# Optimization experiments

Hardware: AMD Instinct MI355X
Metric: run time of the kernel (lower is better)

Reference implementation:

```python
import jax, jax.numpy as jnp
import numpy as np

B, S, D, H = 2, 2048, 1024, 16
DH = D // H  # head dim = 64


def _split_heads(x):
    # [B,S,D] -> [B,H,S,DH]
    return x.reshape(B, S, H, DH).transpose(0, 2, 1, 3)


def setup_inputs() -> dict:
    key = jax.random.key(0)
    ks = jax.random.split(key, 14)
    sc = 1.0 / np.sqrt(D)
    p = {"hidden_states": jax.random.normal(ks[0], (B, S, D), jnp.float32)}
    names = ["Wq", "Wk1", "Wk2", "Wv1", "Wv2", "Wd"]
    for i, n in enumerate(names):
        p[n] = jax.random.normal(ks[1 + 2 * i], (D, D), jnp.float32) * sc
        p["b" + n[1:]] = jax.random.normal(ks[2 + 2 * i], (D,), jnp.float32) * 0.02
    return p


def reference(hidden_states, Wq, bq, Wk1, bk1, Wk2, bk2, Wv1, bv1, Wv2, bv2, Wd, bd):
    q = _split_heads(hidden_states @ Wq + bq)
    k1 = _split_heads(hidden_states @ Wk1 + bk1)
    k2 = _split_heads(hidden_states @ Wk2 + bk2)
    v1 = _split_heads(hidden_states @ Wv1 + bv1)
    v2 = _split_heads(hidden_states @ Wv2 + bv2)

    scores = jnp.einsum("bhqd,bhkd->bhqk", q, k1) / np.sqrt(DH)
    causal = jnp.tril(jnp.ones((S, S), dtype=bool))  # True = keep
    scores = jnp.where(causal, scores, -jnp.inf)
    probs = jax.nn.softmax(scores, axis=-1)

    ctx = jnp.einsum("bhqk,bhkd->bhqd", probs, v1)          # [B,H,S,DH]
    ctx = jnp.einsum("bhqd,bhkd->bhqk", ctx, k2)            # [B,H,S,S]
    ctx = jnp.einsum("bhqk,bhkd->bhqd", ctx, v2)            # [B,H,S,DH]

    ctx = ctx.transpose(0, 2, 1, 3).reshape(B, S, D)
    return ctx @ Wd + bd
```

## Files before the change

kernel.cpp:

```cpp
#include <hip/hip_runtime.h>
#include <hip/hip_bf16.h>

typedef __bf16 bf16x8 __attribute__((ext_vector_type(8)));
typedef float f32x4 __attribute__((ext_vector_type(4)));
using bf16 = __hip_bfloat16;

#define SEQ 2048
#define DM 1024
#define NH 16
#define DH 64
#define NBH 32
#define MR 4096

#define WAITBAR(N) asm volatile("s_waitcnt vmcnt(" #N ")\n\ts_barrier" ::: "memory")

static __device__ __forceinline__ void async_cp16(const void* gsrc, void* ldsdst) {
  __builtin_amdgcn_global_load_lds((__attribute__((address_space(1))) void*)gsrc,
                                   (__attribute__((address_space(3))) void*)ldsdst, 16, 0, 0);
}

static __device__ __forceinline__ unsigned short f2bfu(float f) {
  bf16 h = __float2bfloat16(f);
  unsigned short u; __builtin_memcpy(&u, &h, 2); return u;
}
static __device__ __forceinline__ unsigned int pack_bf2(float lo, float hi) {
  return (unsigned int)f2bfu(lo) | ((unsigned int)f2bfu(hi) << 16);
}

__global__ __launch_bounds__(256) void cast_x(const float* __restrict__ X, bf16* __restrict__ Xb) {
  long g = ((long)blockIdx.x * 256 + threadIdx.x) * 8;
  float4 a = *(const float4*)(X + g);
  float4 b = *(const float4*)(X + g + 4);
  unsigned short u[8];
  u[0]=f2bfu(a.x); u[1]=f2bfu(a.y); u[2]=f2bfu(a.z); u[3]=f2bfu(a.w);
  u[4]=f2bfu(b.x); u[5]=f2bfu(b.y); u[6]=f2bfu(b.z); u[7]=f2bfu(b.w);
  uint4 o; __builtin_memcpy(&o, u, 16);
  *(uint4*)(Xb + g) = o;
}

struct WPtrs { const float* w[6]; };

__global__ __launch_bounds__(256) void transpose_cast_w(WPtrs wp, bf16* __restrict__ WtAll) {
  const int z = blockIdx.z;
  const float* W = wp.w[z];
  bf16* Wt = WtAll + (long)z * DM * DM;
  __shared__ float Ts[32][33];
  int n0 = blockIdx.x * 32, k0 = blockIdx.y * 32;
  int tx = threadIdx.x, ty = threadIdx.y;
#pragma unroll
  for (int it = 0; it < 4; ++it)
    Ts[ty + 8*it][tx] = W[(long)(k0 + ty + 8*it) * DM + n0 + tx];
  __syncthreads();
#pragma unroll
  for (int it = 0; it < 4; ++it)
    Wt[(long)(n0 + ty + 8*it) * DM + k0 + tx] = __float2bfloat16(Ts[tx][ty + 8*it]);
}

struct ProjArgs {
  const float* bias[5];
  bf16* out[5];
};

__global__ __launch_bounds__(256, 2) void gemm_proj(const bf16* __restrict__ A,
                                                    const bf16* __restrict__ WtAll, ProjArgs p) {
  __shared__ alignas(16) bf16 SM[36864];
  bf16* As = SM;
  bf16* Bs = SM + 12288;
  const int tid = threadIdx.x;
  const int bid = blockIdx.x;
  const int mt = bid & 31, nt = bid >> 5;
  const int m0 = mt * 128;
  const int z = nt >> 2;
  const int n0z = (nt & 3) * 256;
  const bf16* Bt = WtAll + (long)z * DM * DM + (long)n0z * DM;

  const int wave = tid >> 6, lane = tid & 63, l15 = lane & 15, l4 = lane >> 4;
  const int wm = wave >> 1, wn = wave & 1;

  const int prow = tid >> 2;
  const int cc = (tid & 3) ^ ((prow >> 1) & 3);
  const bf16* sA0 = A  + (long)(m0 + prow) * DM + cc * 8;
  const bf16* sA1 = sA0 + 64L * DM;
  const bf16* sB0 = Bt + (long)prow * DM + cc * 8;
  const bf16* sB1 = sB0 + 64L * DM;
  const bf16* sB2 = sB0 + 128L * DM;
  const bf16* sB3 = sB0 + 192L * DM;
  char* dA = (char*)As + wave * 1024;
  char* dB = (char*)Bs + wave * 1024;

#define PSTAGE(KT_, BUF_) do {                                  \
    int ko_ = (KT_) * 32;                                       \
    async_cp16(sA0 + ko_, dA + (BUF_) * 8192);                  \
    async_cp16(sA1 + ko_, dA + (BUF_) * 8192 + 4096);           \
    async_cp16(sB0 + ko_, dB + (BUF_) * 16384);                 \
    async_cp16(sB1 + ko_, dB + (BUF_) * 16384 + 4096);          \
    async_cp16(sB2 + ko_, dB + (BUF_) * 16384 + 8192);          \
    async_cp16(sB3 + ko_, dB + (BUF_) * 16384 + 12288);         \
  } while (0)

  const int slot8 = (l4 ^ ((l15 >> 1) & 3)) * 8;
  const int arow = wm * 64 + l15;
  const int brow = wn * 128 + l15;
  f32x4 acc[4][8] = {};

#define PCOMPUTE(BUF_) do {                                                        \
    const bf16* ab_ = As + (BUF_) * 4096;                                          \
    const bf16* bb_ = Bs + (BUF_) * 8192;                                          \
    bf16x8 af_[4], bq_[8];                                                         \
    _Pragma("unroll")                                                              \
    for (int i = 0; i < 4; ++i) af_[i] = *(const bf16x8*)(ab_ + (arow + i * 16) * 32 + slot8); \
    _Pragma("unroll")                                                              \
    for (int j = 0; j < 8; ++j) bq_[j] = *(const bf16x8*)(bb_ + (brow + j * 16) * 32 + slot8); \
    _Pragma("unroll")                                                              \
    for (int i = 0; i < 4; ++i)                                                    \
      _Pragma("unroll")                                                            \
      for (int j = 0; j < 8; ++j)                                                  \
        acc[i][j] = __builtin_amdgcn_mfma_f32_16x16x32_bf16(af_[i], bq_[j], acc[i][j], 0, 0, 0); \
  } while (0)

  PSTAGE(0, 0);
  PSTAGE(1, 1);
  int buf = 0;
#pragma unroll 1
  for (int k = 0; k < 31; ++k) {
    WAITBAR(6);
    if (k < 30) {
      int nb = buf + 2; if (nb > 2) nb -= 3;
      PSTAGE(k + 2, nb);
    }
    PCOMPUTE(buf);
    ++buf; if (buf > 2) buf = 0;
  }
  WAITBAR(0);
  PCOMPUTE(buf);
#undef PSTAGE
#undef PCOMPUTE

  const float* bias = p.bias[z];
  bf16* out = p.out[z];
  float bv[8];
#pragma unroll
  for (int j = 0; j < 8; ++j) bv[j] = bias[n0z + wn * 128 + j * 16 + l15];

  if (z < 2) {
    const float scale = (z == 0) ? 0.125f * 1.44269504f : 1.0f;
#pragma unroll
    for (int i = 0; i < 4; ++i)
#pragma unroll
      for (int j = 0; j < 8; ++j)
#pragma unroll
        for (int r = 0; r < 4; ++r) {
          int m = m0 + wm * 64 + i * 16 + l4 * 4 + r;
          int n = n0z + wn * 128 + j * 16 + l15;
          int b = m >> 11, s = m & 2047, hh = n >> 6, d = n & 63;
          out[((long)((b * NH + hh) * SEQ + s)) * DH + d] =
              __float2bfloat16((acc[i][j][r] + bv[j]) * scale);
        }
  } else {
    __syncthreads();
    bf16* Os = SM;
#pragma unroll
    for (int i = 0; i < 4; ++i)
#pragma unroll
      for (int j = 0; j < 8; ++j)
#pragma unroll
        for (int r = 0; r < 4; ++r) {
          int nl = wn * 128 + j * 16 + l15;
          int ml = wm * 64 + i * 16 + l4 * 4 + r;
          Os[nl * 136 + ml] = __float2bfloat16(acc[i][j][r] + bv[j]);
        }
    __syncthreads();
    {
      int nl = tid;
      int ng = n0z + nl;
      int hh = ng >> 6, d = ng & 63;
      int b = m0 >> 11, s0 = m0 & 2047;
      bf16* op = out + ((long)((b * NH + hh) * DH + d)) * SEQ + s0;
#pragma unroll
      for (int u = 0; u < 16; ++u)
        *(bf16x8*)(op + u * 8) = *(const bf16x8*)(Os + nl * 136 + u * 8);
    }
  }
}

static __device__ __forceinline__ void gemm_core128(
    const bf16* __restrict__ A, const bf16* __restrict__ Bt,
    bf16* As, bf16* Bs, f32x4 (&acc)[4][4], int m0, int tid)
{
  const int wave = tid >> 6, lane = tid & 63, l15 = lane & 15, l4 = lane >> 4;
  const int wm = wave >> 1, wn = wave & 1;
  const int r0 = tid >> 2;
  const int c0 = (tid & 3) ^ ((r0 >> 1) & 3);
  const bf16* srcA0 = A + (long)(m0 + r0) * DM + c0 * 8;
  const bf16* srcA1 = A + (long)(m0 + r0 + 64) * DM + c0 * 8;
  const bf16* srcB0 = Bt + (long)r0 * DM + c0 * 8;
  const bf16* srcB1 = Bt + (long)(r0 + 64) * DM + c0 * 8;
  char* dstA = (char*)As + wave * 1024;
  char* dstB = (char*)Bs + wave * 1024;

#define STAGE(KT_, BUF_) do {                                   \
    int ko_ = (KT_) * 32;                                       \
    int bo_ = (BUF_) * 8192;                                    \
    async_cp16(srcA0 + ko_, dstA + bo_);                        \
    async_cp16(srcA1 + ko_, dstA + bo_ + 4096);                 \
    async_cp16(srcB0 + ko_, dstB + bo_);                        \
    async_cp16(srcB1 + ko_, dstB + bo_ + 4096);                 \
  } while (0)

  const int slot8 = (l4 ^ ((l15 >> 1) & 3)) * 8;
  const int arow = wm * 64 + l15;
  const int brow = wn * 64 + l15;

#define COMPUTE(BUF_) do {                                                         \
    const bf16* ab_ = As + (BUF_) * 4096;                                          \
    const bf16* bb_ = Bs + (BUF_) * 4096;                                          \
    bf16x8 af_[4], bq_[4];                                                         \
    _Pragma("unroll")                                                              \
    for (int i = 0; i < 4; ++i) af_[i] = *(const bf16x8*)(ab_ + (arow + i * 16) * 32 + slot8); \
    _Pragma("unroll")                                                              \
    for (int j = 0; j < 4; ++j) bq_[j] = *(const bf16x8*)(bb_ + (brow + j * 16) * 32 + slot8); \
    _Pragma("unroll")                                                              \
    for (int i = 0; i < 4; ++i)                                                    \
      _Pragma("unroll")                                                            \
      for (int j = 0; j < 4; ++j)                                                  \
        acc[i][j] = __builtin_amdgcn_mfma_f32_16x16x32_bf16(af_[i], bq_[j], acc[i][j], 0, 0, 0); \
  } while (0)

  STAGE(0, 0);
  STAGE(1, 1);
  int buf = 0;
#pragma unroll 1
  for (int k = 0; k < 31; ++k) {
    WAITBAR(4);
    if (k < 30) {
      int nb = buf + 2; if (nb > 2) nb -= 3;
      STAGE(k + 2, nb);
    }
    COMPUTE(buf);
    ++buf; if (buf > 2) buf = 0;
  }
  WAITBAR(0);
  COMPUTE(buf);
#undef STAGE
#undef COMPUTE
}

__global__ __launch_bounds__(256, 3) void gemm_out(const bf16* __restrict__ A, const bf16* __restrict__ Bt,
                                                   const float* __restrict__ bias, float* __restrict__ out) {
  __shared__ alignas(16) bf16 As[3 * 128 * 32];
  __shared__ alignas(16) bf16 Bs[3 * 128 * 32];
  const int tid = threadIdx.x;
  const int bid = blockIdx.x;
  const int nt = bid & 7, mt = bid >> 3;
  const int m0 = mt * 128, n0 = nt * 128;
  f32x4 acc[4][4] = {};
  gemm_core128(A, Bt + (long)n0 * DM, As, Bs, acc, m0, tid);
  const int wave = tid >> 6, lane = tid & 63, l15 = lane & 15, l4 = lane >> 4;
  const int wm = wave >> 1, wn = wave & 1;
  float bv[4];
#pragma unroll
  for (int j = 0; j < 4; ++j) bv[j] = bias[n0 + wn * 64 + j * 16 + l15];
#pragma unroll
  for (int i = 0; i < 4; ++i)
#pragma unroll
    for (int j = 0; j < 4; ++j)
#pragma unroll
      for (int r = 0; r < 4; ++r) {
        int m = m0 + wm * 64 + i * 16 + l4 * 4 + r;
        int n = n0 + wn * 64 + j * 16 + l15;
        out[(long)m * DM + n] = acc[i][j][r] + bv[j];
      }
}

__global__ __launch_bounds__(256) void m_kernel(
    const bf16* __restrict__ k2t, const bf16* __restrict__ v2t, float* __restrict__ Mbuf)
{
  const int scx = blockIdx.x;
  const int bh = blockIdx.y;
  const int tid = threadIdx.x, wave = tid >> 6, lane = tid & 63, l15 = lane & 15, l4 = lane >> 4;
  const bf16* kp = k2t + (long)bh * DH * SEQ;
  const bf16* vp = v2t + (long)bh * DH * SEQ;
  __shared__ alignas(16) bf16 K2s[64 * 32];
  __shared__ alignas(16) bf16 V2s[64 * 32];
  f32x4 acc[4] = {};
  const int s0 = scx * 256;
  for (int kk = 0; kk < 256; kk += 32) {
    __syncthreads();
    {
      int c = tid, r = c >> 2, pp = c & 3;
      async_cp16(kp + (long)r * SEQ + s0 + kk + pp * 8, K2s + wave * 64 * 8);
      async_cp16(vp + (long)r * SEQ + s0 + kk + pp * 8, V2s + wave * 64 * 8);
    }
    __syncthreads();
    int arow = 16 * wave + l15;
    bf16x8 a = *(const bf16x8*)(K2s + arow * 32 + l4 * 8);
#pragma unroll
    for (int nb = 0; nb < 4; ++nb) {
      int col = nb * 16 + l15;
      bf16x8 b = *(const bf16x8*)(V2s + col * 32 + l4 * 8);
      acc[nb] = __builtin_amdgcn_mfma_f32_16x16x32_bf16(a, b, acc[nb], 0, 0, 0);
    }
  }
  float* Mp = Mbuf + (long)bh * 4096;
#pragma unroll
  for (int nb = 0; nb < 4; ++nb)
#pragma unroll
    for (int r = 0; r < 4; ++r) {
      int row = 16 * wave + l4 * 4 + r;
      int col = nb * 16 + l15;
      atomicAdd(Mp + row * 64 + col, acc[nb][r]);
    }
}

static __device__ __forceinline__ void redist(const unsigned int (&pk)[4][2], bf16x8 (&pb)[2],
                                              int l4, int l15) {
#pragma unroll
  for (int h = 0; h < 2; ++h) {
    unsigned int w4[4];
#pragma unroll
    for (int w = 0; w < 4; ++w) {
      int src = l15 + 16 * (2 * (l4 & 1) + (w >> 1));
      unsigned int va = (unsigned int)__shfl((int)pk[2 * h][w & 1], src);
      unsigned int vb = (unsigned int)__shfl((int)pk[2 * h + 1][w & 1], src);
      w4[w] = (l4 & 2) ? vb : va;
    }
    __builtin_memcpy(&pb[h], w4, 16);
  }
}

__global__ __launch_bounds__(256) void attn_fused(
    const bf16* __restrict__ q,
    const bf16* __restrict__ k1,
    const bf16* __restrict__ v1t,
    const float* __restrict__ Mbuf,
    bf16* __restrict__ ctx2,
    unsigned int* __restrict__ cnt)
{
  const int tid = threadIdx.x, wave = tid >> 6, lane = tid & 63;
  const int l15 = lane & 15, l4 = lane >> 4;

  __shared__ alignas(16) bf16 Ks[2][64 * 64];
  __shared__ alignas(16) bf16 Vs[2][64 * 64];
  __shared__ int ts;

#define STAGE_KV(JJ, BUF) do {                                                     \
    int kv0_ = 64 * (JJ);                                                          \
    int c_ = tid, row_ = c_ >> 3, ch_ = c_ & 7;                                    \
    async_cp16(kp + (long)(kv0_ + row_) * DH + ((ch_ ^ (row_ & 7)) * 8),           \
               (char*)Ks[BUF] + wave * 1024);                                      \
    async_cp16(vp + (long)row_ * SEQ + kv0_ + ((ch_ ^ (row_ & 7)) * 8),            \
               (char*)Vs[BUF] + wave * 1024);                                      \
    c_ = tid + 256; row_ = c_ >> 3; ch_ = c_ & 7;                                  \
    async_cp16(kp + (long)(kv0_ + row_) * DH + ((ch_ ^ (row_ & 7)) * 8),           \
               (char*)Ks[BUF] + 4096 + wave * 1024);                               \
    async_cp16(vp + (long)row_ * SEQ + kv0_ + ((ch_ ^ (row_ & 7)) * 8),            \
               (char*)Vs[BUF] + 4096 + wave * 1024);                               \
  } while (0)

#pragma unroll 1
  for (;;) {
    if (tid == 0) ts = (int)atomicAdd(cnt, 1u);
    __syncthreads();
    const int t = ts;
    if (t >= 1024) break;
    const int tq = 31 - (t >> 5);
    const int bh = t & 31;
    const int bb = bh >> 4, hh = bh & 15;
    const bf16* qp = q   + (long)bh * SEQ * DH;
    const bf16* kp = k1  + (long)bh * SEQ * DH;
    const bf16* vp = v1t + (long)bh * DH * SEQ;
    const float* Mp = Mbuf + (long)bh * 4096;

    bf16x8 mf[4][2];
#pragma unroll
    for (int db = 0; db < 4; ++db)
#pragma unroll
      for (int h = 0; h < 2; ++h) {
        bf16x8 tt;
#pragma unroll
        for (int j = 0; j < 8; ++j)
          tt[j] = (__bf16)Mp[(32 * h + 8 * l4 + j) * 64 + 16 * db + l15];
        mf[db][h] = tt;
      }

    const int Q0 = 64 * tq;
    const int qg = Q0 + 16 * wave + l15;
    const int jmax = tq;

    STAGE_KV(0, 0);

    bf16x8 aq[2];
#pragma unroll
    for (int h = 0; h < 2; ++h)
      aq[h] = *(const bf16x8*)(qp + (long)qg * DH + 32 * h + 8 * l4);

    float m_run = -__builtin_inff(), l_run = 0.f;
    f32x4 acc_o[4] = {};

    __syncthreads();

#pragma unroll 1
    for (int j = 0; j <= jmax; ++j) {
      const int cur = j & 1;
      if (j < jmax) STAGE_KV(j + 1, cur ^ 1);

      f32x4 sc[4] = {};
      __builtin_amdgcn_s_setprio(1);
#pragma unroll
      for (int nb = 0; nb < 4; ++nb) {
        const bf16* krow = Ks[cur] + (16 * nb + l15) * 64;
#pragma unroll
        for (int h = 0; h < 2; ++h) {
          bf16x8 kf = *(const bf16x8*)(krow + (((4 * h + l4) ^ (l15 & 7)) * 8));
          sc[nb] = __builtin_amdgcn_mfma_f32_16x16x32_bf16(kf, aq[h], sc[nb], 0, 0, 0);
        }
      }
      __builtin_amdgcn_s_setprio(0);

      if (j == jmax) {
        const int kv0 = 64 * j;
#pragma unroll
        for (int nb = 0; nb < 4; ++nb)
#pragma unroll
          for (int r = 0; r < 4; ++r)
            if (kv0 + 16 * nb + 4 * l4 + r > qg) sc[nb][r] = -__builtin_inff();
      }

      float tmax = -__builtin_inff();
#pragma unroll
      for (int nb = 0; nb < 4; ++nb)
#pragma unroll
        for (int r = 0; r < 4; ++r) tmax = fmaxf(tmax, sc[nb][r]);
      tmax = fmaxf(tmax, __shfl_xor(tmax, 16));
      tmax = fmaxf(tmax, __shfl_xor(tmax, 32));

      float mnew = m_run;
      if (!__all(tmax <= m_run)) {
        mnew = fmaxf(m_run, tmax);
        float sf = __builtin_amdgcn_exp2f(m_run - mnew);
        m_run = mnew;
        l_run *= sf;
#pragma unroll
        for (int db = 0; db < 4; ++db)
#pragma unroll
          for (int r = 0; r < 4; ++r) acc_o[db][r] *= sf;
      }

      float ssum = 0.f;
      unsigned int pk[4][2];
#pragma unroll
      for (int nb = 0; nb < 4; ++nb)
#pragma unroll
        for (int pr = 0; pr < 2; ++pr) {
          float p0 = __builtin_amdgcn_exp2f(sc[nb][2 * pr]     - m_run);
          float p1 = __builtin_amdgcn_exp2f(sc[nb][2 * pr + 1] - m_run);
          ssum += p0 + p1;
          pk[nb][pr] = pack_bf2(p0, p1);
        }
      ssum += __shfl_xor(ssum, 16);
      ssum += __shfl_xor(ssum, 32);
      l_run += ssum;

      bf16x8 pb[2];
      redist(pk, pb, l4, l15);
      __builtin_amdgcn_s_setprio(1);
#pragma unroll
      for (int db = 0; db < 4; ++db) {
        const bf16* vrow = Vs[cur] + (16 * db + l15) * 64;
#pragma unroll
        for (int h = 0; h < 2; ++h) {
          bf16x8 vf = *(const bf16x8*)(vrow + (((4 * h + l4) ^ (l15 & 7)) * 8));
          acc_o[db] = __builtin_amdgcn_mfma_f32_16x16x32_bf16(vf, pb[h], acc_o[db], 0, 0, 0);
        }
      }
      __builtin_amdgcn_s_setprio(0);
      __syncthreads();
    }

    float invl = __builtin_amdgcn_rcpf(l_run);
    unsigned int ck[4][2];
#pragma unroll
    for (int db = 0; db < 4; ++db)
#pragma unroll
      for (int pr = 0; pr < 2; ++pr)
        ck[db][pr] = pack_bf2(acc_o[db][2 * pr] * invl, acc_o[db][2 * pr + 1] * invl);
    bf16x8 cb[2];
    redist(ck, cb, l4, l15);
    f32x4 o2[4] = {};
#pragma unroll
    for (int db = 0; db < 4; ++db)
#pragma unroll
      for (int h = 0; h < 2; ++h)
        o2[db] = __builtin_amdgcn_mfma_f32_16x16x32_bf16(mf[db][h], cb[h], o2[db], 0, 0, 0);

    bf16* Os = (bf16*)Ks;
#pragma unroll
    for (int db = 0; db < 4; ++db)
#pragma unroll
      for (int r = 0; r < 4; ++r)
        Os[(16 * wave + l15) * 72 + 16 * db + 4 * l4 + r] = __float2bfloat16(o2[db][r]);
    __syncthreads();
    {
      int rr = tid >> 2, cc2 = tid & 3;
      long obase = ((long)(bb * SEQ + Q0 + rr)) * DM + hh * DH + cc2 * 16;
      *(bf16x8*)(ctx2 + obase)     = *(const bf16x8*)(Os + rr * 72 + cc2 * 16);
      *(bf16x8*)(ctx2 + obase + 8) = *(const bf16x8*)(Os + rr * 72 + cc2 * 16 + 8);
    }
  }
#undef STAGE_KV
}

extern "C" void kernel_launch(void* const* d_in, const int* in_sizes, int n_in,
                              void* d_out, int out_size, void* d_ws, size_t ws_size,
                              hipStream_t stream) {
  (void)in_sizes; (void)n_in; (void)out_size; (void)ws_size;
  const float* X = (const float*)d_in[0];
  const float* W[6]    = {(const float*)d_in[1], (const float*)d_in[3], (const float*)d_in[5],
                          (const float*)d_in[7], (const float*)d_in[9], (const float*)d_in[11]};
  const float* bias[6] = {(const float*)d_in[2], (const float*)d_in[4], (const float*)d_in[6],
                          (const float*)d_in[8], (const float*)d_in[10], (const float*)d_in[12]};

  char* ws = (char*)d_ws;
  bf16* Xb  = (bf16*)(ws);
  bf16* Wt  = (bf16*)(ws + (8L  << 20));
  bf16* qB  = (bf16*)(ws + (20L << 20));
  bf16* k1B = (bf16*)(ws + (28L << 20));
  bf16* k2t = (bf16*)(ws + (36L << 20));
  bf16* v1t = (bf16*)(ws + (44L << 20));
  bf16* v2t = (bf16*)(ws + (52L << 20));
  float* Mb = (float*)(ws + (60L << 20));
  unsigned int* cnt = (unsigned int*)(ws + (61L << 20));
  bf16* c2  = Xb;

  cast_x<<<2048, 256, 0, stream>>>(X, Xb);

  WPtrs wp; for (int z = 0; z < 6; ++z) wp.w[z] = W[z];
  transpose_cast_w<<<dim3(32, 32, 6), dim3(32, 8), 0, stream>>>(wp, Wt);

  ProjArgs pa;
  for (int z = 0; z < 5; ++z) pa.bias[z] = bias[z];
  pa.out[0] = qB; pa.out[1] = k1B; pa.out[2] = k2t; pa.out[3] = v1t; pa.out[4] = v2t;
  gemm_proj<<<640, 256, 0, stream>>>(Xb, Wt, pa);

  hipMemsetAsync(Mb, 0, ((size_t)1 << 20) + 64, stream);
  hipMemsetAsync(cnt, 0, 4, stream);
  m_kernel<<<dim3(8, 32), 256, 0, stream>>>(k2t, v2t, Mb);

  attn_fused<<<512, 256, 0, stream>>>(qB, k1B, v1t, Mb, c2, cnt);

  gemm_out<<<256, 256, 0, stream>>>(c2, Wt + 5L * DM * DM, bias[5], (float*)d_out);
}
```

Measured before the change: 171.2 us.

## Rewrite fused attention as per-wave 32-row tiles with 32x32 MFMA and register-streamed K/V

```diff
diff --git a/kernel.cpp b/kernel.cpp
--- a/kernel.cpp
+++ b/kernel.cpp
@@ -3,6 +3,7 @@
 
 typedef __bf16 bf16x8 __attribute__((ext_vector_type(8)));
 typedef float f32x4 __attribute__((ext_vector_type(4)));
+typedef float f32x16 __attribute__((ext_vector_type(16)));
 using bf16 = __hip_bfloat16;
 
 #define SEQ 2048
@@ -312,22 +313,6 @@
     }
 }
 
-static __device__ __forceinline__ void redist(const unsigned int (&pk)[4][2], bf16x8 (&pb)[2],
-                                              int l4, int l15) {
-#pragma unroll
-  for (int h = 0; h < 2; ++h) {
-    unsigned int w4[4];
-#pragma unroll
-    for (int w = 0; w < 4; ++w) {
-      int src = l15 + 16 * (2 * (l4 & 1) + (w >> 1));
-      unsigned int va = (unsigned int)__shfl((int)pk[2 * h][w & 1], src);
-      unsigned int vb = (unsigned int)__shfl((int)pk[2 * h + 1][w & 1], src);
-      w4[w] = (l4 & 2) ? vb : va;
-    }
-    __builtin_memcpy(&pb[h], w4, 16);
-  }
-}
-
 __global__ __launch_bounds__(256) void attn_fused(
     const bf16* __restrict__ q,
     const bf16* __restrict__ k1,
@@ -336,178 +321,207 @@
     bf16* __restrict__ ctx2,
     unsigned int* __restrict__ cnt)
 {
-  const int tid = threadIdx.x, wave = tid >> 6, lane = tid & 63;
-  const int l15 = lane & 15, l4 = lane >> 4;
-
-  __shared__ alignas(16) bf16 Ks[2][64 * 64];
-  __shared__ alignas(16) bf16 Vs[2][64 * 64];
-  __shared__ int ts;
-
-#define STAGE_KV(JJ, BUF) do {                                                     \
-    int kv0_ = 64 * (JJ);                                                          \
-    int c_ = tid, row_ = c_ >> 3, ch_ = c_ & 7;                                    \
-    async_cp16(kp + (long)(kv0_ + row_) * DH + ((ch_ ^ (row_ & 7)) * 8),           \
-               (char*)Ks[BUF] + wave * 1024);                                      \
-    async_cp16(vp + (long)row_ * SEQ + kv0_ + ((ch_ ^ (row_ & 7)) * 8),            \
-               (char*)Vs[BUF] + wave * 1024);                                      \
-    c_ = tid + 256; row_ = c_ >> 3; ch_ = c_ & 7;                                  \
-    async_cp16(kp + (long)(kv0_ + row_) * DH + ((ch_ ^ (row_ & 7)) * 8),           \
-               (char*)Ks[BUF] + 4096 + wave * 1024);                               \
-    async_cp16(vp + (long)row_ * SEQ + kv0_ + ((ch_ ^ (row_ & 7)) * 8),            \
-               (char*)Vs[BUF] + 4096 + wave * 1024);                               \
-  } while (0)
+  const int tid = threadIdx.x, wv = tid >> 6, lane = tid & 63;
+  const int l31 = lane & 31, l5 = lane >> 5;
+  const bool hi = (l5 != 0);
+  __shared__ alignas(16) bf16 TRS[4][2048];
+  bf16* trs = TRS[wv];
 
 #pragma unroll 1
   for (;;) {
-    if (tid == 0) ts = (int)atomicAdd(cnt, 1u);
-    __syncthreads();
-    const int t = ts;
-    if (t >= 1024) break;
-    const int tq = 31 - (t >> 5);
-    const int bh = t & 31;
+    int tv = 0;
+    if (lane == 0) tv = (int)atomicAdd(cnt, 1u);
+    const int t = __shfl(tv, 0);
+    if (t >= 2048) break;
+    const int bh = t >> 6;
+    const int tq = 63 - (t & 63);
     const int bb = bh >> 4, hh = bh & 15;
+    const int q0 = 32 * tq;
+    const int qg = q0 + l31;
+    const int jmax = tq >> 1;
+
     const bf16* qp = q   + (long)bh * SEQ * DH;
     const bf16* kp = k1  + (long)bh * SEQ * DH;
     const bf16* vp = v1t + (long)bh * DH * SEQ;
-    const float* Mp = Mbuf + (long)bh * 4096;
-
-    bf16x8 mf[4][2];
-#pragma unroll
-    for (int db = 0; db < 4; ++db)
-#pragma unroll
-      for (int h = 0; h < 2; ++h) {
-        bf16x8 tt;
-#pragma unroll
-        for (int j = 0; j < 8; ++j)
-          tt[j] = (__bf16)Mp[(32 * h + 8 * l4 + j) * 64 + 16 * db + l15];
-        mf[db][h] = tt;
-      }
-
-    const int Q0 = 64 * tq;
-    const int qg = Q0 + 16 * wave + l15;
-    const int jmax = tq;
-
-    STAGE_KV(0, 0);
-
-    bf16x8 aq[2];
-#pragma unroll
-    for (int h = 0; h < 2; ++h)
-      aq[h] = *(const bf16x8*)(qp + (long)qg * DH + 32 * h + 8 * l4);
-
+
+    bf16x8 aq0 = *(const bf16x8*)(qp + (long)qg * DH +  0 + 8 * l5);
+    bf16x8 aq1 = *(const bf16x8*)(qp + (long)qg * DH + 16 + 8 * l5);
+    bf16x8 aq2 = *(const bf16x8*)(qp + (long)qg * DH + 32 + 8 * l5);
+    bf16x8 aq3 = *(const bf16x8*)(qp + (long)qg * DH + 48 + 8 * l5);
+
+    const bf16* klane = kp + (long)l31 * DH + 8 * l5;
+    const bf16* vlane = vp + (long)l31 * SEQ + 8 * l5;
+
+    f32x16 acc0 = {}, acc1 = {};
     float m_run = -__builtin_inff(), l_run = 0.f;
-    f32x4 acc_o[4] = {};
-
-    __syncthreads();
+
+    bf16x8 kf[2][4], vf[2][4];
+#pragma unroll
+    for (int kt = 0; kt < 2; ++kt)
+#pragma unroll
+      for (int kk = 0; kk < 4; ++kk)
+        kf[kt][kk] = *(const bf16x8*)(klane + (long)(32 * kt) * DH + 16 * kk);
+#pragma unroll
+    for (int dt = 0; dt < 2; ++dt)
+#pragma unroll
+      for (int ks = 0; ks < 4; ++ks)
+        vf[dt][ks] = *(const bf16x8*)(vlane + (long)(32 * dt) * SEQ + 16 * ks);
 
 #pragma unroll 1
     for (int j = 0; j <= jmax; ++j) {
-      const int cur = j & 1;
-      if (j < jmax) STAGE_KV(j + 1, cur ^ 1);
-
-      f32x4 sc[4] = {};
-      __builtin_amdgcn_s_setprio(1);
-#pragma unroll
-      for (int nb = 0; nb < 4; ++nb) {
-        const bf16* krow = Ks[cur] + (16 * nb + l15) * 64;
-#pragma unroll
-        for (int h = 0; h < 2; ++h) {
-          bf16x8 kf = *(const bf16x8*)(krow + (((4 * h + l4) ^ (l15 & 7)) * 8));
-          sc[nb] = __builtin_amdgcn_mfma_f32_16x16x32_bf16(kf, aq[h], sc[nb], 0, 0, 0);
+      const int kv0 = 64 * j;
+
+      f32x16 s0 = {}, s1 = {};
+      s0 = __builtin_amdgcn_mfma_f32_32x32x16_bf16(kf[0][0], aq0, s0, 0, 0, 0);
+      s1 = __builtin_amdgcn_mfma_f32_32x32x16_bf16(kf[1][0], aq0, s1, 0, 0, 0);
+      s0 = __builtin_amdgcn_mfma_f32_32x32x16_bf16(kf[0][1], aq1, s0, 0, 0, 0);
+      s1 = __builtin_amdgcn_mfma_f32_32x32x16_bf16(kf[1][1], aq1, s1, 0, 0, 0);
+      s0 = __builtin_amdgcn_mfma_f32_32x32x16_bf16(kf[0][2], aq2, s0, 0, 0, 0);
+      s1 = __builtin_amdgcn_mfma_f32_32x32x16_bf16(kf[1][2], aq2, s1, 0, 0, 0);
+      s0 = __builtin_amdgcn_mfma_f32_32x32x16_bf16(kf[0][3], aq3, s0, 0, 0, 0);
+      s1 = __builtin_amdgcn_mfma_f32_32x32x16_bf16(kf[1][3], aq3, s1, 0, 0, 0);
+
+      if (j < jmax) {
+        const bf16* kn = klane + (long)(64 * (j + 1)) * DH;
+#pragma unroll
+        for (int kt = 0; kt < 2; ++kt)
+#pragma unroll
+          for (int kk = 0; kk < 4; ++kk)
+            kf[kt][kk] = *(const bf16x8*)(kn + (long)(32 * kt) * DH + 16 * kk);
+      }
+
+      if (j == jmax) {
+#pragma unroll
+        for (int r = 0; r < 16; ++r) {
+          int kvo = 4 * l5 + (r & 3) + 8 * (r >> 2);
+          if (kv0 + kvo      > qg) s0[r] = -__builtin_inff();
+          if (kv0 + 32 + kvo > qg) s1[r] = -__builtin_inff();
         }
       }
-      __builtin_amdgcn_s_setprio(0);
-
-      if (j == jmax) {
-        const int kv0 = 64 * j;
-#pragma unroll
-        for (int nb = 0; nb < 4; ++nb)
-#pragma unroll
-          for (int r = 0; r < 4; ++r)
-            if (kv0 + 16 * nb + 4 * l4 + r > qg) sc[nb][r] = -__builtin_inff();
-      }
 
       float tmax = -__builtin_inff();
 #pragma unroll
-      for (int nb = 0; nb < 4; ++nb)
-#pragma unroll
-        for (int r = 0; r < 4; ++r) tmax = fmaxf(tmax, sc[nb][r]);
-      tmax = fmaxf(tmax, __shfl_xor(tmax, 16));
+      for (int r = 0; r < 16; ++r) tmax = fmaxf(tmax, fmaxf(s0[r], s1[r]));
       tmax = fmaxf(tmax, __shfl_xor(tmax, 32));
 
-      float mnew = m_run;
       if (!__all(tmax <= m_run)) {
-        mnew = fmaxf(m_run, tmax);
+        float mnew = fmaxf(m_run, tmax);
         float sf = __builtin_amdgcn_exp2f(m_run - mnew);
         m_run = mnew;
         l_run *= sf;
 #pragma unroll
-        for (int db = 0; db < 4; ++db)
-#pragma unroll
-          for (int r = 0; r < 4; ++r) acc_o[db][r] *= sf;
+        for (int r = 0; r < 16; ++r) { acc0[r] *= sf; acc1[r] *= sf; }
       }
 
       float ssum = 0.f;
-      unsigned int pk[4][2];
-#pragma unroll
-      for (int nb = 0; nb < 4; ++nb)
-#pragma unroll
-        for (int pr = 0; pr < 2; ++pr) {
-          float p0 = __builtin_amdgcn_exp2f(sc[nb][2 * pr]     - m_run);
-          float p1 = __builtin_amdgcn_exp2f(sc[nb][2 * pr + 1] - m_run);
-          ssum += p0 + p1;
-          pk[nb][pr] = pack_bf2(p0, p1);
-        }
-      ssum += __shfl_xor(ssum, 16);
+      unsigned int w0[8], w1[8];
+#pragma unroll
+      for (int i = 0; i < 8; ++i) {
+        float a0 = __builtin_amdgcn_exp2f(s0[2 * i]     - m_run);
+        float a1 = __builtin_amdgcn_exp2f(s0[2 * i + 1] - m_run);
+        float b0 = __builtin_amdgcn_exp2f(s1[2 * i]     - m_run);
+        float b1 = __builtin_amdgcn_exp2f(s1[2 * i + 1] - m_run);
+        ssum += (a0 + a1) + (b0 + b1);
+        w0[i] = pack_bf2(a0, a1);
+        w1[i] = pack_bf2(b0, b1);
+      }
       ssum += __shfl_xor(ssum, 32);
       l_run += ssum;
 
-      bf16x8 pb[2];
-      redist(pk, pb, l4, l15);
-      __builtin_amdgcn_s_setprio(1);
-#pragma unroll
-      for (int db = 0; db < 4; ++db) {
-        const bf16* vrow = Vs[cur] + (16 * db + l15) * 64;
-#pragma unroll
-        for (int h = 0; h < 2; ++h) {
-          bf16x8 vf = *(const bf16x8*)(vrow + (((4 * h + l4) ^ (l15 & 7)) * 8));
-          acc_o[db] = __builtin_amdgcn_mfma_f32_16x16x32_bf16(vf, pb[h], acc_o[db], 0, 0, 0);
+      unsigned int x0[8], x1[8];
+#pragma unroll
+      for (int i = 0; i < 8; ++i) {
+        x0[i] = (unsigned int)__shfl_xor((int)w0[i], 32);
+        x1[i] = (unsigned int)__shfl_xor((int)w1[i], 32);
+      }
+
+#pragma unroll
+      for (int ks = 0; ks < 4; ++ks) {
+        const int qq = 4 * (ks & 1);
+        unsigned int jw[4];
+        if (ks < 2) {
+          jw[0] = hi ? x0[qq + 2] : w0[qq];
+          jw[1] = hi ? x0[qq + 3] : w0[qq + 1];
+          jw[2] = hi ? w0[qq + 2] : x0[qq];
+          jw[3] = hi ? w0[qq + 3] : x0[qq + 1];
+        } else {
+          jw[0] = hi ? x1[qq + 2] : w1[qq];
+          jw[1] = hi ? x1[qq + 3] : w1[qq + 1];
+          jw[2] = hi ? w1[qq + 2] : x1[qq];
+          jw[3] = hi ? w1[qq + 3] : x1[qq + 1];
         }
-      }
-      __builtin_amdgcn_s_setprio(0);
-      __syncthreads();
-    }
-
+        bf16x8 pb; __builtin_memcpy(&pb, jw, 16);
+        acc0 = __builtin_amdgcn_mfma_f32_32x32x16_bf16(vf[0][ks], pb, acc0, 0, 0, 0);
+        acc1 = __builtin_amdgcn_mfma_f32_32x32x16_bf16(vf[1][ks], pb, acc1, 0, 0, 0);
+      }
+
+      if (j < jmax) {
+        const bf16* vn = vlane + 64 * (j + 1);
+#pragma unroll
+        for (int dt = 0; dt < 2; ++dt)
+#pragma unroll
+          for (int ks = 0; ks < 4; ++ks)
+            vf[dt][ks] = *(const bf16x8*)(vn + (long)(32 * dt) * SEQ + 16 * ks);
+      }
+    }
+
+    const float* Mp = Mbuf + (long)bh * 4096;
     float invl = __builtin_amdgcn_rcpf(l_run);
-    unsigned int ck[4][2];
-#pragma unroll
-    for (int db = 0; db < 4; ++db)
-#pragma unroll
-      for (int pr = 0; pr < 2; ++pr)
-        ck[db][pr] = pack_bf2(acc_o[db][2 * pr] * invl, acc_o[db][2 * pr + 1] * invl);
-    bf16x8 cb[2];
-    redist(ck, cb, l4, l15);
-    f32x4 o2[4] = {};
-#pragma unroll
-    for (int db = 0; db < 4; ++db)
-#pragma unroll
-      for (int h = 0; h < 2; ++h)
-        o2[db] = __builtin_amdgcn_mfma_f32_16x16x32_bf16(mf[db][h], cb[h], o2[db], 0, 0, 0);
-
-    bf16* Os = (bf16*)Ks;
-#pragma unroll
-    for (int db = 0; db < 4; ++db)
-#pragma unroll
-      for (int r = 0; r < 4; ++r)
-        Os[(16 * wave + l15) * 72 + 16 * db + 4 * l4 + r] = __float2bfloat16(o2[db][r]);
-    __syncthreads();
+    unsigned int cw0[8], cw1[8], cx0[8], cx1[8];
+#pragma unroll
+    for (int i = 0; i < 8; ++i) {
+      cw0[i] = pack_bf2(acc0[2 * i] * invl, acc0[2 * i + 1] * invl);
+      cw1[i] = pack_bf2(acc1[2 * i] * invl, acc1[2 * i + 1] * invl);
+    }
+#pragma unroll
+    for (int i = 0; i < 8; ++i) {
+      cx0[i] = (unsigned int)__shfl_xor((int)cw0[i], 32);
+      cx1[i] = (unsigned int)__shfl_xor((int)cw1[i], 32);
+    }
+
+    f32x16 o0 = {}, o1 = {};
+#pragma unroll
+    for (int ks = 0; ks < 4; ++ks) {
+      const int qq = 4 * (ks & 1);
+      unsigned int jw[4];
+      if (ks < 2) {
+        jw[0] = hi ? cx0[qq + 2] : cw0[qq];
+        jw[1] = hi ? cx0[qq + 3] : cw0[qq + 1];
+        jw[2] = hi ? cw0[qq + 2] : cx0[qq];
+        jw[3] = hi ? cw0[qq + 3] : cx0[qq + 1];
+      } else {
+        jw[0] = hi ? cx1[qq + 2] : cw1[qq];
+        jw[1] = hi ? cx1[qq + 3] : cw1[qq + 1];
+        jw[2] = hi ? cw1[qq + 2] : cx1[qq];
+        jw[3] = hi ? cw1[qq + 3] : cx1[qq + 1];
+      }
+      bf16x8 cb; __builtin_memcpy(&cb, jw, 16);
+      bf16x8 mA0, mA1;
+#pragma unroll
+      for (int jj = 0; jj < 8; ++jj) {
+        mA0[jj] = (__bf16)Mp[(16 * ks + 8 * l5 + jj) * 64 + l31];
+        mA1[jj] = (__bf16)Mp[(16 * ks + 8 * l5 + jj) * 64 + 32 + l31];
+      }
+      o0 = __builtin_amdgcn_mfma_f32_32x32x16_bf16(mA0, cb, o0, 0, 0, 0);
+      o1 = __builtin_amdgcn_mfma_f32_32x32x16_bf16(mA1, cb, o1, 0, 0, 0);
+    }
+
+#pragma unroll
+    for (int i = 0; i < 8; ++i) {
+      int dd = 4 * l5 + 2 * (i & 1) + 8 * (i >> 1);
+      *(unsigned int*)((char*)trs + l31 * 128 + dd * 2) = pack_bf2(o0[2 * i], o0[2 * i + 1]);
+      *(unsigned int*)((char*)trs + l31 * 128 + (dd + 32) * 2) = pack_bf2(o1[2 * i], o1[2 * i + 1]);
+    }
+    asm volatile("s_waitcnt lgkmcnt(0)" ::: "memory");
     {
-      int rr = tid >> 2, cc2 = tid & 3;
-      long obase = ((long)(bb * SEQ + Q0 + rr)) * DM + hh * DH + cc2 * 16;
-      *(bf16x8*)(ctx2 + obase)     = *(const bf16x8*)(Os + rr * 72 + cc2 * 16);
-      *(bf16x8*)(ctx2 + obase + 8) = *(const bf16x8*)(Os + rr * 72 + cc2 * 16 + 8);
-    }
+      long obase = ((long)(bb * SEQ + q0 + l31)) * DM + hh * DH + l5 * 32;
+      const bf16* src = trs + l31 * 64 + l5 * 32;
+#pragma unroll
+      for (int u = 0; u < 4; ++u)
+        *(bf16x8*)(ctx2 + obase + 8 * u) = *(const bf16x8*)(src + 8 * u);
+    }
+    asm volatile("s_waitcnt lgkmcnt(0) vmcnt(0)" ::: "memory");
   }
-#undef STAGE_KV
 }
 
 extern "C" void kernel_launch(void* const* d_in, const int* in_sizes, int n_in,
@@ -542,11 +556,11 @@
   pa.out[0] = qB; pa.out[1] = k1B; pa.out[2] = k2t; pa.out[3] = v1t; pa.out[4] = v2t;
   gemm_proj<<<640, 256, 0, stream>>>(Xb, Wt, pa);
 
-  hipMemsetAsync(Mb, 0, ((size_t)1 << 20) + 64, stream);
+  hipMemsetAsync(Mb, 0, (size_t)NBH * 4096 * 4, stream);
   hipMemsetAsync(cnt, 0, 4, stream);
   m_kernel<<<dim3(8, 32), 256, 0, stream>>>(k2t, v2t, Mb);
 
-  attn_fused<<<512, 256, 0, stream>>>(qB, k1B, v1t, Mb, c2, cnt);
+  attn_fused<<<256, 256, 0, stream>>>(qB, k1B, v1t, Mb, c2, cnt);
 
   gemm_out<<<256, 256, 0, stream>>>(c2, Wt + 5L * DM * DM, bias[5], (float*)d_out);
 }
```

New measurement: 210.0 us. 1.23x slower.
